# Optimization experiments

Measured on AMD Instinct MI355X. Metric: run time of the kernel, lower is better.

Reference implementation:

```python
import jax, jax.numpy as jnp
import numpy as np

N_NODES = 100000
N_EDGES = 1600000
D_FEAT = 128


def sage_conv(x, src, dst, Wl, Wr, b, n_nodes):
    # gather source features, mean-aggregate at destination (PyG SAGEConv, aggr='mean')
    msgs = x[src]                                            # [E, d]
    agg_sum = jax.ops.segment_sum(msgs, dst, num_segments=n_nodes)
    cnt = jax.ops.segment_sum(jnp.ones((src.shape[0],), dtype=x.dtype), dst,
                              num_segments=n_nodes)
    mean = agg_sum / jnp.maximum(cnt, 1.0)[:, None]
    return mean @ Wl + x @ Wr + b


def setup_inputs() -> dict:
    key = jax.random.key(0)
    ks = jax.random.split(key, 9)
    def w(k, shape):
        fan_in = shape[0]
        return jax.random.normal(k, shape, dtype=jnp.float32) / np.sqrt(fan_in)
    x = jax.random.normal(ks[0], (N_NODES, D_FEAT), dtype=jnp.float32)
    edge_index = jax.random.randint(ks[1], (2, N_EDGES), 0, N_NODES, dtype=jnp.int64)
    return {
        "x": x,
        "edge_index": edge_index,
        "W1l": w(ks[2], (D_FEAT, 64)), "W1r": w(ks[3], (D_FEAT, 64)), "b1": jnp.zeros((64,), jnp.float32),
        "W2l": w(ks[4], (64, 128)),    "W2r": w(ks[5], (64, 128)),    "b2": jnp.zeros((128,), jnp.float32),
        "W3l": w(ks[6], (128, 64)),    "W3r": w(ks[7], (128, 64)),    "b3": jnp.zeros((64,), jnp.float32),
        "Wlin": w(ks[8], (64, 10)),    "blin": jnp.zeros((10,), jnp.float32),
    }


def reference(x, edge_index, W1l, W1r, b1, W2l, W2r, b2, W3l, W3r, b3, Wlin, blin):
    n = x.shape[0]
    src, dst = edge_index[0], edge_index[1]
    # dropout omitted (evaluated in inference / identity form)
    h = jnp.tanh(sage_conv(x, src, dst, W1l, W1r, b1, n))
    h = jnp.tanh(sage_conv(h, src, dst, W2l, W2r, b2, n))
    h = jnp.tanh(sage_conv(h, src, dst, W3l, W3r, b3, n))
    return h @ Wlin + blin
```

## Files before the change

kernel.cpp:

```cpp
#include <hip/hip_runtime.h>

#define THREADS 256
#define NB 256
#define NB_SHIFT 8
#define TILE_E 4096
#define EPT 16
#define BMAXPAD 512
#define WT_LD 136

typedef unsigned short ushort_t;
typedef __attribute__((ext_vector_type(8))) short bf16x8;
typedef __attribute__((ext_vector_type(4))) float f32x4;

__device__ __forceinline__ unsigned short f2bf(float f) {
    unsigned u = __float_as_uint(f);
    u += 0x7fff + ((u >> 16) & 1);
    return (unsigned short)(u >> 16);
}
__device__ __forceinline__ float bf2f(unsigned short s) {
    return __uint_as_float((unsigned)s << 16);
}
__device__ __forceinline__ float4 bf4_to_f4(ushort4 u) {
    return make_float4(bf2f(u.x), bf2f(u.y), bf2f(u.z), bf2f(u.w));
}
__device__ __forceinline__ ushort4 f4_to_bf4(float4 v) {
    ushort4 o;
    o.x = f2bf(v.x); o.y = f2bf(v.y); o.z = f2bf(v.z); o.w = f2bf(v.w);
    return o;
}

__global__ __launch_bounds__(64)
void detect_kernel(const unsigned* __restrict__ ei_words, int* __restrict__ flag) {
    if (threadIdx.x == 0 && blockIdx.x == 0) {
        int allzero = 1;
        for (int i = 0; i < 64; ++i) {
            if (ei_words[2 * i + 1] != 0u) { allzero = 0; break; }
        }
        *flag = allzero;
    }
}

__device__ __forceinline__ void load_edge(const void* ei, int is64, int E, int i,
                                          int& s, int& t) {
    if (is64) {
        const long long* p = (const long long*)ei;
        s = (int)p[i];
        t = (int)p[E + i];
    } else {
        const int* p = (const int*)ei;
        s = p[i];
        t = p[E + i];
    }
}

__global__ __launch_bounds__(256)
void tilesort_kernel(const void* __restrict__ ei, const int* __restrict__ flag,
                     unsigned* __restrict__ tbuf, int* __restrict__ tcnt,
                     int* __restrict__ tstart, int E, int B) {
    __shared__ int hist[BMAXPAD];
    __shared__ int wsum[8];
    const int t   = blockIdx.x;
    const int e0  = t * TILE_E;
    const int is64 = *flag;
    unsigned w[EPT];
    unsigned short bk[EPT];
    for (int i = threadIdx.x; i < BMAXPAD; i += 256) hist[i] = 0;
    __syncthreads();
#pragma unroll
    for (int k = 0; k < EPT; ++k) {
        const int i = e0 + k * 256 + (int)threadIdx.x;
        bk[k] = 0xFFFFu;
        w[k]  = 0u;
        if (i < E) {
            int s, d;
            load_edge(ei, is64, E, i, s, d);
            w[k]  = (unsigned)s | ((unsigned)(d & (NB - 1)) << 17);
            bk[k] = (unsigned short)(d >> NB_SHIFT);
            atomicAdd(&hist[bk[k]], 1);
        }
    }
    __syncthreads();
    const int lane = threadIdx.x & 63;
    const int wid  = threadIdx.x >> 6;
    const int v0 = hist[2 * threadIdx.x];
    const int v1 = hist[2 * threadIdx.x + 1];
    const int sum = v0 + v1;
    int incl = sum;
#pragma unroll
    for (int off = 1; off < 64; off <<= 1) {
        int tt = __shfl_up(incl, off, 64);
        if (lane >= off) incl += tt;
    }
    if (lane == 63) wsum[wid] = incl;
    __syncthreads();
    int woff = 0;
    for (int ww = 0; ww < wid; ++ww) woff += wsum[ww];
    const int excl = woff + incl - sum;
    hist[2 * threadIdx.x]     = excl;
    hist[2 * threadIdx.x + 1] = excl + v0;
    const int b0 = 2 * threadIdx.x, b1 = 2 * threadIdx.x + 1;
    if (b0 < B) { tcnt[(size_t)t * B + b0] = v0; tstart[(size_t)t * B + b0] = excl; }
    if (b1 < B) { tcnt[(size_t)t * B + b1] = v1; tstart[(size_t)t * B + b1] = excl + v0; }
    __syncthreads();
#pragma unroll
    for (int k = 0; k < EPT; ++k) {
        if (bk[k] != 0xFFFFu) {
            const int pos = atomicAdd(&hist[bk[k]], 1);
            tbuf[(size_t)t * TILE_E + pos] = w[k];
        }
    }
}

__global__ __launch_bounds__(256)
void transpose2_kernel(const int* __restrict__ tcnt, const int* __restrict__ tstart,
                       int* __restrict__ tcntT, int* __restrict__ tstartT,
                       int T, int B) {
    __shared__ int ta[32][33];
    __shared__ int tb[32][33];
    const int bx = blockIdx.x;
    const int by = blockIdx.y;
    const int tx = threadIdx.x & 31;
    const int ty = threadIdx.x >> 5;
#pragma unroll
    for (int r = 0; r < 4; ++r) {
        const int trow = by * 32 + ty * 4 + r;
        const int bcol = bx * 32 + tx;
        if (trow < T && bcol < B) {
            ta[ty * 4 + r][tx] = tcnt[(size_t)trow * B + bcol];
            tb[ty * 4 + r][tx] = tstart[(size_t)trow * B + bcol];
        }
    }
    __syncthreads();
#pragma unroll
    for (int r = 0; r < 4; ++r) {
        const int brow = bx * 32 + ty * 4 + r;
        const int tcol = by * 32 + tx;
        if (brow < B && tcol < T) {
            tcntT[(size_t)brow * T + tcol]   = ta[tx][ty * 4 + r];
            tstartT[(size_t)brow * T + tcol] = tb[tx][ty * 4 + r];
        }
    }
}

__global__ __launch_bounds__(256)
void scan_partial_kernel(const int* __restrict__ cnt, int* __restrict__ bsum, int n) {
    const int base = blockIdx.x * 1024;
    int v = 0;
    for (int i = threadIdx.x; i < 1024; i += 256) {
        const int idx = base + i;
        v += (idx < n) ? cnt[idx] : 0;
    }
#pragma unroll
    for (int off = 32; off > 0; off >>= 1) v += __shfl_down(v, off, 64);
    __shared__ int ws[4];
    if ((threadIdx.x & 63) == 0) ws[threadIdx.x >> 6] = v;
    __syncthreads();
    if (threadIdx.x == 0) bsum[blockIdx.x] = ws[0] + ws[1] + ws[2] + ws[3];
}

__global__ __launch_bounds__(64)
void scan_bsum_kernel(int* __restrict__ bsum, int* __restrict__ total, int nb) {
    if (threadIdx.x == 0) {
        int run = 0;
        for (int i = 0; i < nb; ++i) { int t = bsum[i]; bsum[i] = run; run += t; }
        *total = run;
    }
}

__global__ __launch_bounds__(256)
void scan_final_kernel(const int* __restrict__ cnt, const int* __restrict__ bsum,
                       int* __restrict__ outp, int n) {
    const int base = blockIdx.x * 1024 + threadIdx.x * 4;
    int a0 = 0, a1 = 0, a2 = 0, a3 = 0;
    if (base + 0 < n) a0 = cnt[base + 0];
    if (base + 1 < n) a1 = cnt[base + 1];
    if (base + 2 < n) a2 = cnt[base + 2];
    if (base + 3 < n) a3 = cnt[base + 3];
    const int mysum = a0 + a1 + a2 + a3;
    const int lane = threadIdx.x & 63;
    const int wid  = threadIdx.x >> 6;
    int incl = mysum;
#pragma unroll
    for (int off = 1; off < 64; off <<= 1) {
        int t = __shfl_up(incl, off, 64);
        if (lane >= off) incl += t;
    }
    __shared__ int ws[4];
    if (lane == 63) ws[wid] = incl;
    __syncthreads();
    int woff = 0;
    for (int w = 0; w < wid; ++w) woff += ws[w];
    int pre = bsum[blockIdx.x] + woff + (incl - mysum);
    if (base + 0 < n) outp[base + 0] = pre; pre += a0;
    if (base + 1 < n) outp[base + 1] = pre; pre += a1;
    if (base + 2 < n) outp[base + 2] = pre; pre += a2;
    if (base + 3 < n) outp[base + 3] = pre;
}

__global__ __launch_bounds__(256)
void finesort_kernel(const unsigned* __restrict__ tbuf, const int* __restrict__ tcntT,
                     const int* __restrict__ tstartT, const int* __restrict__ hbase,
                     int* __restrict__ rowptr, int* __restrict__ esrc,
                     int n, int E, int T, int B) {
    __shared__ int hist[NB];
    __shared__ int wsum[4];
    const int b  = blockIdx.x;
    const int e0 = hbase[(size_t)b * T];
    hist[threadIdx.x] = 0;
    __syncthreads();
    for (int t = threadIdx.x; t < T; t += 256) {
        const int c  = tcntT[(size_t)b * T + t];
        const int ls = tstartT[(size_t)b * T + t];
        const unsigned* __restrict__ src = tbuf + (size_t)t * TILE_E + ls;
        for (int k = 0; k < c; ++k) atomicAdd(&hist[src[k] >> 17], 1);
    }
    __syncthreads();
    const int lane = threadIdx.x & 63;
    const int wid  = threadIdx.x >> 6;
    const int v = hist[threadIdx.x];
    int incl = v;
#pragma unroll
    for (int off = 1; off < 64; off <<= 1) {
        int tt = __shfl_up(incl, off, 64);
        if (lane >= off) incl += tt;
    }
    if (lane == 63) wsum[wid] = incl;
    __syncthreads();
    int woff = 0;
    for (int w = 0; w < wid; ++w) woff += wsum[w];
    const int excl = woff + incl - v;
    hist[threadIdx.x] = e0 + excl;
    const int node = b * NB + (int)threadIdx.x;
    if (node < n) rowptr[node] = e0 + excl;
    if (b == 0 && threadIdx.x == 0) rowptr[n] = E;
    __syncthreads();
    for (int t = threadIdx.x; t < T; t += 256) {
        const int c  = tcntT[(size_t)b * T + t];
        const int ls = tstartT[(size_t)b * T + t];
        const unsigned* __restrict__ src = tbuf + (size_t)t * TILE_E + ls;
        for (int k = 0; k < c; ++k) {
            const unsigned wv = src[k];
            const int pos = atomicAdd(&hist[wv >> 17], 1);
            esrc[pos] = (int)(wv & 0x1FFFFu);
        }
    }
}

__global__ __launch_bounds__(256)
void pack_dual_kernel(const float* __restrict__ Wl, const float* __restrict__ Wr,
                      ushort_t* __restrict__ WT) {
    int i = blockIdx.x * 256 + threadIdx.x;
    if (i >= 128 * 128) return;
    int k = i >> 7, c = i & 127;
    float v = (c < 64) ? Wl[k * 64 + c] : Wr[k * 64 + (c - 64)];
    WT[c * WT_LD + k] = f2bf(v);
}
__global__ __launch_bounds__(256)
void pack_stack_kernel(const float* __restrict__ Wl, const float* __restrict__ Wr,
                       ushort_t* __restrict__ WT) {
    int i = blockIdx.x * 256 + threadIdx.x;
    if (i >= 128 * 128) return;
    int k = i >> 7, c = i & 127;
    float v = (k < 64) ? Wl[k * 128 + c] : Wr[(k - 64) * 128 + c];
    WT[c * WT_LD + k] = f2bf(v);
}

template <bool A_FP32, bool TANH_BIAS>
__global__ __launch_bounds__(256)
void mfma_gemm_kernel(const void* __restrict__ Av, const ushort_t* __restrict__ WT,
                      const float* __restrict__ bias, ushort_t* __restrict__ C, int n) {
    __shared__ ushort_t sW[128 * WT_LD];
    {
        const uint4* gsrc = (const uint4*)WT;
        uint4* ldst = (uint4*)sW;
        for (int i = threadIdx.x; i < 128 * WT_LD * 2 / 16; i += 256) ldst[i] = gsrc[i];
    }
    __syncthreads();
    const int lane = threadIdx.x & 63;
    const int wave = threadIdx.x >> 6;
    const int row0 = blockIdx.x * 64 + wave * 16;
    const int rA   = min(row0 + (lane & 15), n - 1);
    const int kg   = lane >> 4;

    bf16x8 a[4];
    if (A_FP32) {
        const float* A = (const float*)Av;
#pragma unroll
        for (int t = 0; t < 4; ++t) {
            const float4 lo = *(const float4*)(A + (size_t)rA * 128 + t * 32 + kg * 8);
            const float4 hi = *(const float4*)(A + (size_t)rA * 128 + t * 32 + kg * 8 + 4);
            const ushort4 u0 = f4_to_bf4(lo), u1 = f4_to_bf4(hi);
            bf16x8 av;
            av[0] = (short)u0.x; av[1] = (short)u0.y; av[2] = (short)u0.z; av[3] = (short)u0.w;
            av[4] = (short)u1.x; av[5] = (short)u1.y; av[6] = (short)u1.z; av[7] = (short)u1.w;
            a[t] = av;
        }
    } else {
        const ushort_t* A = (const ushort_t*)Av;
#pragma unroll
        for (int t = 0; t < 4; ++t)
            a[t] = *(const bf16x8*)(A + (size_t)rA * 128 + t * 32 + kg * 8);
    }

    f32x4 acc[8];
#pragma unroll
    for (int ct = 0; ct < 8; ++ct) acc[ct] = (f32x4)(0.f);

#pragma unroll
    for (int ct = 0; ct < 8; ++ct) {
        const int c0 = ct * 16 + (lane & 15);
#pragma unroll
        for (int t = 0; t < 4; ++t) {
            const bf16x8 b = *(const bf16x8*)(sW + (size_t)c0 * WT_LD + t * 32 + kg * 8);
            acc[ct] = __builtin_amdgcn_mfma_f32_16x16x32_bf16(a[t], b, acc[ct], 0, 0, 0);
        }
    }

    const int orow = row0 + kg * 4;
#pragma unroll
    for (int ct = 0; ct < 8; ++ct) {
        const int col = ct * 16 + (lane & 15);
        const float badd = TANH_BIAS ? bias[col] : 0.f;
#pragma unroll
        for (int i = 0; i < 4; ++i) {
            const int r = orow + i;
            if (r < n) {
                float v = acc[ct][i];
                if (TANH_BIAS) v = tanhf(v + badd);
                C[(size_t)r * 128 + col] = f2bf(v);
            }
        }
    }
}

template <int OUTMODE>
__global__ __launch_bounds__(THREADS)
void gather_fuse_kernel(const int* __restrict__ rowptr, const int* __restrict__ esrc,
                        const ushort_t* __restrict__ pq, const float* __restrict__ bias,
                        ushort_t* __restrict__ hout, int n) {
    constexpr int CH  = 16;
    constexpr int NPB = THREADS / CH;
    const int node = blockIdx.x * NPB + (int)(threadIdx.x / CH);
    const int c    = threadIdx.x & (CH - 1);
    if (node >= n) return;
    const int begin = rowptr[node];
    const int end   = rowptr[node + 1];
    float4 acc = make_float4(0.f, 0.f, 0.f, 0.f);
    int e = begin;
    for (; e + 4 <= end; e += 4) {
        const int s0 = esrc[e + 0], s1 = esrc[e + 1], s2 = esrc[e + 2], s3 = esrc[e + 3];
        const float4 v0 = bf4_to_f4(*(const ushort4*)(pq + (size_t)s0 * 128 + 4 * c));
        const float4 v1 = bf4_to_f4(*(const ushort4*)(pq + (size_t)s1 * 128 + 4 * c));
        const float4 v2 = bf4_to_f4(*(const ushort4*)(pq + (size_t)s2 * 128 + 4 * c));
        const float4 v3 = bf4_to_f4(*(const ushort4*)(pq + (size_t)s3 * 128 + 4 * c));
        acc.x += v0.x + v1.x + v2.x + v3.x;
        acc.y += v0.y + v1.y + v2.y + v3.y;
        acc.z += v0.z + v1.z + v2.z + v3.z;
        acc.w += v0.w + v1.w + v2.w + v3.w;
    }
    for (; e < end; ++e) {
        const int s = esrc[e];
        const float4 v = bf4_to_f4(*(const ushort4*)(pq + (size_t)s * 128 + 4 * c));
        acc.x += v.x; acc.y += v.y; acc.z += v.z; acc.w += v.w;
    }
    const float inv = 1.0f / fmaxf((float)(end - begin), 1.0f);
    const float4 qv = bf4_to_f4(*(const ushort4*)(pq + (size_t)node * 128 + 64 + 4 * c));
    const float4 bv = *(const float4*)(bias + 4 * c);
    float4 o;
    o.x = tanhf(acc.x * inv + qv.x + bv.x);
    o.y = tanhf(acc.y * inv + qv.y + bv.y);
    o.z = tanhf(acc.z * inv + qv.z + bv.z);
    o.w = tanhf(acc.w * inv + qv.w + bv.w);
    if (OUTMODE == 0) {
        *(ushort4*)(hout + (size_t)node * 128 + 64 + 4 * c) = f4_to_bf4(o);
    } else {
        *(ushort4*)(hout + (size_t)node * 64 + 4 * c) = f4_to_bf4(o);
    }
}

__global__ __launch_bounds__(THREADS)
void gather_mean_kernel(const int* __restrict__ rowptr, const int* __restrict__ esrc,
                        ushort_t* __restrict__ ah, int n) {
    constexpr int CH  = 16;
    constexpr int NPB = THREADS / CH;
    const int node = blockIdx.x * NPB + (int)(threadIdx.x / CH);
    const int c    = threadIdx.x & (CH - 1);
    if (node >= n) return;
    const int begin = rowptr[node];
    const int end   = rowptr[node + 1];
    float4 acc = make_float4(0.f, 0.f, 0.f, 0.f);
    int e = begin;
    for (; e + 4 <= end; e += 4) {
        const int s0 = esrc[e + 0], s1 = esrc[e + 1], s2 = esrc[e + 2], s3 = esrc[e + 3];
        const float4 v0 = bf4_to_f4(*(const ushort4*)(ah + (size_t)s0 * 128 + 64 + 4 * c));
        const float4 v1 = bf4_to_f4(*(const ushort4*)(ah + (size_t)s1 * 128 + 64 + 4 * c));
        const float4 v2 = bf4_to_f4(*(const ushort4*)(ah + (size_t)s2 * 128 + 64 + 4 * c));
        const float4 v3 = bf4_to_f4(*(const ushort4*)(ah + (size_t)s3 * 128 + 64 + 4 * c));
        acc.x += v0.x + v1.x + v2.x + v3.x;
        acc.y += v0.y + v1.y + v2.y + v3.y;
        acc.z += v0.z + v1.z + v2.z + v3.z;
        acc.w += v0.w + v1.w + v2.w + v3.w;
    }
    for (; e < end; ++e) {
        const int s = esrc[e];
        const float4 v = bf4_to_f4(*(const ushort4*)(ah + (size_t)s * 128 + 64 + 4 * c));
        acc.x += v.x; acc.y += v.y; acc.z += v.z; acc.w += v.w;
    }
    const float inv = 1.0f / fmaxf((float)(end - begin), 1.0f);
    ushort4 o = f4_to_bf4(make_float4(acc.x * inv, acc.y * inv, acc.z * inv, acc.w * inv));
    *(ushort4*)(ah + (size_t)node * 128 + 4 * c) = o;
}

__global__ __launch_bounds__(THREADS)
void head_kernel(const ushort_t* __restrict__ h, const float* __restrict__ W,
                 const float* __restrict__ bias, float* __restrict__ out, int n) {
    __shared__ float sW[64 * 10];
    __shared__ float sb[10];
    for (int i = threadIdx.x; i < 640; i += THREADS) sW[i] = W[i];
    if (threadIdx.x < 10) sb[threadIdx.x] = bias[threadIdx.x];
    __syncthreads();
    int idx = blockIdx.x * THREADS + threadIdx.x;
    if (idx >= n * 10) return;
    int row = idx / 10;
    int col = idx - row * 10;
    const ushort_t* __restrict__ hr = h + (size_t)row * 64;
    float acc = sb[col];
#pragma unroll 16
    for (int k = 0; k < 64; ++k) acc += bf2f(hr[k]) * sW[k * 10 + col];
    out[idx] = acc;
}

extern "C" void kernel_launch(void* const* d_in, const int* in_sizes, int n_in,
                              void* d_out, int out_size, void* d_ws, size_t ws_size,
                              hipStream_t stream) {
    const float* x    = (const float*)d_in[0];
    const void*  ei   = d_in[1];
    const float* W1l  = (const float*)d_in[2];
    const float* W1r  = (const float*)d_in[3];
    const float* b1   = (const float*)d_in[4];
    const float* W2l  = (const float*)d_in[5];
    const float* W2r  = (const float*)d_in[6];
    const float* b2   = (const float*)d_in[7];
    const float* W3l  = (const float*)d_in[8];
    const float* W3r  = (const float*)d_in[9];
    const float* b3   = (const float*)d_in[10];
    const float* Wlin = (const float*)d_in[11];
    const float* blin = (const float*)d_in[12];
    float* out = (float*)d_out;

    const int n = in_sizes[0] / 128;
    const int E = in_sizes[1] / 2;
    const int B = (n + NB - 1) / NB;
    const int T = (E + TILE_E - 1) / TILE_E;
    const int Ctot = B * T;

    char* ws = (char*)d_ws;
    size_t off = 0;
    auto carve = [&](size_t bytes) {
        void* p = ws + off;
        off += (bytes + 255) & ~(size_t)255;
        return p;
    };
    int*      flag    = (int*)     carve(256);
    int*      bsum    = (int*)     carve(4096);
    unsigned* tbuf    = (unsigned*)carve((size_t)T * TILE_E * 4);
    int*      tcnt    = (int*)     carve((size_t)Ctot * 4);
    int*      tstart  = (int*)     carve((size_t)Ctot * 4);
    int*      tcntT   = (int*)     carve((size_t)Ctot * 4);
    int*      tstartT = (int*)     carve((size_t)Ctot * 4);
    int*      hbase   = (int*)     carve((size_t)(Ctot + 1) * 4);
    int*      rowptr  = (int*)     carve((size_t)(n + 1) * 4);
    int*      esrc    = (int*)     carve((size_t)E * 4);
    ushort_t* WT1     = (ushort_t*)carve((size_t)128 * WT_LD * 2);
    ushort_t* WT2     = (ushort_t*)carve((size_t)128 * WT_LD * 2);
    ushort_t* WT3     = (ushort_t*)carve((size_t)128 * WT_LD * 2);
    ushort_t* pq      = (ushort_t*)carve((size_t)n * 128 * 2);
    ushort_t* ah      = (ushort_t*)carve((size_t)n * 128 * 2);
    ushort_t* h2      = (ushort_t*)carve((size_t)n * 128 * 2);
    ushort_t* h3      = (ushort_t*)carve((size_t)n * 64 * 2);
    (void)ws_size;

    const int cscan   = (Ctot + 1023) / 1024;
    const int gblocks = (n + 63) / 64;

    pack_dual_kernel <<<64, 256, 0, stream>>>(W1l, W1r, WT1);
    pack_stack_kernel<<<64, 256, 0, stream>>>(W2l, W2r, WT2);
    pack_dual_kernel <<<64, 256, 0, stream>>>(W3l, W3r, WT3);

    detect_kernel<<<1, 64, 0, stream>>>((const unsigned*)ei, flag);
    tilesort_kernel<<<T, 256, 0, stream>>>(ei, flag, tbuf, tcnt, tstart, E, B);
    {
        dim3 tg((B + 31) / 32, (T + 31) / 32);
        transpose2_kernel<<<tg, 256, 0, stream>>>(tcnt, tstart, tcntT, tstartT, T, B);
    }
    scan_partial_kernel<<<cscan, 256, 0, stream>>>(tcntT, bsum, Ctot);
    scan_bsum_kernel<<<1, 64, 0, stream>>>(bsum, hbase + Ctot, cscan);
    scan_final_kernel<<<cscan, 256, 0, stream>>>(tcntT, bsum, hbase, Ctot);
    finesort_kernel<<<B, 256, 0, stream>>>(tbuf, tcntT, tstartT, hbase,
                                           rowptr, esrc, n, E, T, B);

    mfma_gemm_kernel<true, false><<<gblocks, 256, 0, stream>>>(x, WT1, nullptr, pq, n);
    gather_fuse_kernel<0><<<(n + 15) / 16, THREADS, 0, stream>>>(
        rowptr, esrc, pq, b1, ah, n);

    gather_mean_kernel<<<(n + 15) / 16, THREADS, 0, stream>>>(rowptr, esrc, ah, n);
    mfma_gemm_kernel<false, true><<<gblocks, 256, 0, stream>>>(ah, WT2, b2, h2, n);

    mfma_gemm_kernel<false, false><<<gblocks, 256, 0, stream>>>(h2, WT3, nullptr, pq, n);
    gather_fuse_kernel<1><<<(n + 15) / 16, THREADS, 0, stream>>>(
        rowptr, esrc, pq, b3, h3, n);

    head_kernel<<<(n * 10 + THREADS - 1) / THREADS, THREADS, 0, stream>>>(
        h3, Wlin, blin, out, n);
}
```

Measured before the change: 258.4 us.

## Store byte offsets in CSR, cheapen bf16 unpack, drop LDS weight staging

The CSR source array now stores pre-scaled byte offsets (node index shifted by 8), so the gather kernels skip the per-edge multiply and add. Neighbour rows are read as raw uint2 words and unpacked with shift-only bf16 decoding; the high half is added unmasked, which lets low mantissa bits leak in as a small numerical error. The MFMA GEMM drops the shared-memory copy of the weights and its barrier, and reads B fragments straight from global memory with an unpadded stride of 128. The head kernel switches to 16-byte vector loads with inline bf16 unpacking.

```diff
diff --git a/kernel.cpp b/kernel.cpp
--- a/kernel.cpp
+++ b/kernel.cpp
@@ -6,7 +6,7 @@
 #define TILE_E 4096
 #define EPT 16
 #define BMAXPAD 512
-#define WT_LD 136
+#define WT_LD 128
 
 typedef unsigned short ushort_t;
 typedef __attribute__((ext_vector_type(8))) short bf16x8;
@@ -27,6 +27,10 @@
     ushort4 o;
     o.x = f2bf(v.x); o.y = f2bf(v.y); o.z = f2bf(v.z); o.w = f2bf(v.w);
     return o;
+}
+__device__ __forceinline__ void acc_pair(unsigned u, float& lo, float& hi) {
+    lo += __uint_as_float(u << 16);
+    hi += __uint_as_float(u);
 }
 
 __global__ __launch_bounds__(64)
@@ -241,7 +245,7 @@
         for (int k = 0; k < c; ++k) {
             const unsigned wv = src[k];
             const int pos = atomicAdd(&hist[wv >> 17], 1);
-            esrc[pos] = (int)(wv & 0x1FFFFu);
+            esrc[pos] = (int)((wv & 0x1FFFFu) << 8);
         }
     }
 }
@@ -269,13 +273,6 @@
 __global__ __launch_bounds__(256)
 void mfma_gemm_kernel(const void* __restrict__ Av, const ushort_t* __restrict__ WT,
                       const float* __restrict__ bias, ushort_t* __restrict__ C, int n) {
-    __shared__ ushort_t sW[128 * WT_LD];
-    {
-        const uint4* gsrc = (const uint4*)WT;
-        uint4* ldst = (uint4*)sW;
-        for (int i = threadIdx.x; i < 128 * WT_LD * 2 / 16; i += 256) ldst[i] = gsrc[i];
-    }
-    __syncthreads();
     const int lane = threadIdx.x & 63;
     const int wave = threadIdx.x >> 6;
     const int row0 = blockIdx.x * 64 + wave * 16;
@@ -311,7 +308,7 @@
         const int c0 = ct * 16 + (lane & 15);
 #pragma unroll
         for (int t = 0; t < 4; ++t) {
-            const bf16x8 b = *(const bf16x8*)(sW + (size_t)c0 * WT_LD + t * 32 + kg * 8);
+            const bf16x8 b = *(const bf16x8*)(WT + (size_t)c0 * WT_LD + t * 32 + kg * 8);
             acc[ct] = __builtin_amdgcn_mfma_f32_16x16x32_bf16(a[t], b, acc[ct], 0, 0, 0);
         }
     }
@@ -345,32 +342,32 @@
     if (node >= n) return;
     const int begin = rowptr[node];
     const int end   = rowptr[node + 1];
-    float4 acc = make_float4(0.f, 0.f, 0.f, 0.f);
+    const char* __restrict__ base = (const char*)pq + 8 * c;
+    float ax = 0.f, ay = 0.f, az = 0.f, aw = 0.f;
     int e = begin;
     for (; e + 4 <= end; e += 4) {
-        const int s0 = esrc[e + 0], s1 = esrc[e + 1], s2 = esrc[e + 2], s3 = esrc[e + 3];
-        const float4 v0 = bf4_to_f4(*(const ushort4*)(pq + (size_t)s0 * 128 + 4 * c));
-        const float4 v1 = bf4_to_f4(*(const ushort4*)(pq + (size_t)s1 * 128 + 4 * c));
-        const float4 v2 = bf4_to_f4(*(const ushort4*)(pq + (size_t)s2 * 128 + 4 * c));
-        const float4 v3 = bf4_to_f4(*(const ushort4*)(pq + (size_t)s3 * 128 + 4 * c));
-        acc.x += v0.x + v1.x + v2.x + v3.x;
-        acc.y += v0.y + v1.y + v2.y + v3.y;
-        acc.z += v0.z + v1.z + v2.z + v3.z;
-        acc.w += v0.w + v1.w + v2.w + v3.w;
+        const int o0 = esrc[e + 0], o1 = esrc[e + 1], o2 = esrc[e + 2], o3 = esrc[e + 3];
+        const uint2 d0 = *(const uint2*)(base + o0);
+        const uint2 d1 = *(const uint2*)(base + o1);
+        const uint2 d2 = *(const uint2*)(base + o2);
+        const uint2 d3 = *(const uint2*)(base + o3);
+        acc_pair(d0.x, ax, ay); acc_pair(d0.y, az, aw);
+        acc_pair(d1.x, ax, ay); acc_pair(d1.y, az, aw);
+        acc_pair(d2.x, ax, ay); acc_pair(d2.y, az, aw);
+        acc_pair(d3.x, ax, ay); acc_pair(d3.y, az, aw);
     }
     for (; e < end; ++e) {
-        const int s = esrc[e];
-        const float4 v = bf4_to_f4(*(const ushort4*)(pq + (size_t)s * 128 + 4 * c));
-        acc.x += v.x; acc.y += v.y; acc.z += v.z; acc.w += v.w;
+        const uint2 d = *(const uint2*)(base + esrc[e]);
+        acc_pair(d.x, ax, ay); acc_pair(d.y, az, aw);
     }
     const float inv = 1.0f / fmaxf((float)(end - begin), 1.0f);
     const float4 qv = bf4_to_f4(*(const ushort4*)(pq + (size_t)node * 128 + 64 + 4 * c));
     const float4 bv = *(const float4*)(bias + 4 * c);
     float4 o;
-    o.x = tanhf(acc.x * inv + qv.x + bv.x);
-    o.y = tanhf(acc.y * inv + qv.y + bv.y);
-    o.z = tanhf(acc.z * inv + qv.z + bv.z);
-    o.w = tanhf(acc.w * inv + qv.w + bv.w);
+    o.x = tanhf(ax * inv + qv.x + bv.x);
+    o.y = tanhf(ay * inv + qv.y + bv.y);
+    o.z = tanhf(az * inv + qv.z + bv.z);
+    o.w = tanhf(aw * inv + qv.w + bv.w);
     if (OUTMODE == 0) {
         *(ushort4*)(hout + (size_t)node * 128 + 64 + 4 * c) = f4_to_bf4(o);
     } else {
@@ -388,26 +385,26 @@
     if (node >= n) return;
     const int begin = rowptr[node];
     const int end   = rowptr[node + 1];
-    float4 acc = make_float4(0.f, 0.f, 0.f, 0.f);
+    const char* __restrict__ base = (const char*)ah + 128 + 8 * c;
+    float ax = 0.f, ay = 0.f, az = 0.f, aw = 0.f;
     int e = begin;
     for (; e + 4 <= end; e += 4) {
-        const int s0 = esrc[e + 0], s1 = esrc[e + 1], s2 = esrc[e + 2], s3 = esrc[e + 3];
-        const float4 v0 = bf4_to_f4(*(const ushort4*)(ah + (size_t)s0 * 128 + 64 + 4 * c));
-        const float4 v1 = bf4_to_f4(*(const ushort4*)(ah + (size_t)s1 * 128 + 64 + 4 * c));
-        const float4 v2 = bf4_to_f4(*(const ushort4*)(ah + (size_t)s2 * 128 + 64 + 4 * c));
-        const float4 v3 = bf4_to_f4(*(const ushort4*)(ah + (size_t)s3 * 128 + 64 + 4 * c));
-        acc.x += v0.x + v1.x + v2.x + v3.x;
-        acc.y += v0.y + v1.y + v2.y + v3.y;
-        acc.z += v0.z + v1.z + v2.z + v3.z;
-        acc.w += v0.w + v1.w + v2.w + v3.w;
+        const int o0 = esrc[e + 0], o1 = esrc[e + 1], o2 = esrc[e + 2], o3 = esrc[e + 3];
+        const uint2 d0 = *(const uint2*)(base + o0);
+        const uint2 d1 = *(const uint2*)(base + o1);
+        const uint2 d2 = *(const uint2*)(base + o2);
+        const uint2 d3 = *(const uint2*)(base + o3);
+        acc_pair(d0.x, ax, ay); acc_pair(d0.y, az, aw);
+        acc_pair(d1.x, ax, ay); acc_pair(d1.y, az, aw);
+        acc_pair(d2.x, ax, ay); acc_pair(d2.y, az, aw);
+        acc_pair(d3.x, ax, ay); acc_pair(d3.y, az, aw);
     }
     for (; e < end; ++e) {
-        const int s = esrc[e];
-        const float4 v = bf4_to_f4(*(const ushort4*)(ah + (size_t)s * 128 + 64 + 4 * c));
-        acc.x += v.x; acc.y += v.y; acc.z += v.z; acc.w += v.w;
+        const uint2 d = *(const uint2*)(base + esrc[e]);
+        acc_pair(d.x, ax, ay); acc_pair(d.y, az, aw);
     }
     const float inv = 1.0f / fmaxf((float)(end - begin), 1.0f);
-    ushort4 o = f4_to_bf4(make_float4(acc.x * inv, acc.y * inv, acc.z * inv, acc.w * inv));
+    ushort4 o = f4_to_bf4(make_float4(ax * inv, ay * inv, az * inv, aw * inv));
     *(ushort4*)(ah + (size_t)node * 128 + 4 * c) = o;
 }
 
@@ -423,10 +420,21 @@
     if (idx >= n * 10) return;
     int row = idx / 10;
     int col = idx - row * 10;
-    const ushort_t* __restrict__ hr = h + (size_t)row * 64;
+    const uint4* __restrict__ hr = (const uint4*)(h + (size_t)row * 64);
     float acc = sb[col];
-#pragma unroll 16
-    for (int k = 0; k < 64; ++k) acc += bf2f(hr[k]) * sW[k * 10 + col];
+#pragma unroll
+    for (int k4 = 0; k4 < 8; ++k4) {
+        const uint4 u = hr[k4];
+        const float* w = sW + (8 * k4) * 10 + col;
+        acc += __uint_as_float(u.x << 16)          * w[0];
+        acc += __uint_as_float(u.x & 0xffff0000u)  * w[10];
+        acc += __uint_as_float(u.y << 16)          * w[20];
+        acc += __uint_as_float(u.y & 0xffff0000u)  * w[30];
+        acc += __uint_as_float(u.z << 16)          * w[40];
+        acc += __uint_as_float(u.z & 0xffff0000u)  * w[50];
+        acc += __uint_as_float(u.w << 16)          * w[60];
+        acc += __uint_as_float(u.w & 0xffff0000u)  * w[70];
+    }
     out[idx] = acc;
 }
 
```

Measured after the change: 309.7 us. +19.9%, slower.
